# Performance work log

Measured on AMD Instinct MI355X. Metric: run time of the kernel, lower is better.

## Reference

```python
import jax, jax.numpy as jnp
import numpy as np

N = 100000   # total nodes (batched graphs)
E = 800000   # random edges (self-loops appended -> E+N total)
G = 2000     # number of graphs in batch
H = 4        # heads per GAT layer
D = 64       # hidden_size (per-head out dim)
IN = 64      # in_feats
EXTRA = 8    # extra graph-level feats
HID = H * D  # 256


def setup_inputs() -> dict:
    key = jax.random.key(0)
    ks = jax.random.split(key, 24)
    s = 0.5  # init std used in the torch module
    feats_node = jax.random.normal(ks[0], (N, IN), jnp.float32)
    feats_graph = jax.random.normal(ks[1], (G, EXTRA), jnp.float32)
    # edges + self loops (DGL GATConv requires no zero-in-degree nodes)
    src = jnp.concatenate([jax.random.randint(ks[2], (E,), 0, N), jnp.arange(N)])
    dst = jnp.concatenate([jax.random.randint(ks[3], (E,), 0, N), jnp.arange(N)])
    node_gid = jnp.sort(jax.random.randint(ks[4], (N,), 0, G))
    # GAT layer 1
    W1 = jax.random.normal(ks[5], (IN, HID), jnp.float32) * s
    al1 = jax.random.normal(ks[6], (H, D), jnp.float32) * s
    ar1 = jax.random.normal(ks[7], (H, D), jnp.float32) * s
    b1 = jnp.zeros((HID,), jnp.float32)
    # GAT layer 2
    W2 = jax.random.normal(ks[8], (HID, HID), jnp.float32) * s
    al2 = jax.random.normal(ks[9], (H, D), jnp.float32) * s
    ar2 = jax.random.normal(ks[10], (H, D), jnp.float32) * s
    b2 = jnp.zeros((HID,), jnp.float32)
    # WeightedAverage readout score
    Ws = jax.random.normal(ks[11], (HID, 1), jnp.float32) * s
    bs = jnp.zeros((1,), jnp.float32)
    # MLP: 264 -> 128 -> 64 -> 1 with SELU
    Wm1 = jax.random.normal(ks[12], (HID + EXTRA, 2 * D), jnp.float32) * s
    bm1 = jnp.zeros((2 * D,), jnp.float32)
    Wm2 = jax.random.normal(ks[13], (2 * D, D), jnp.float32) * s
    bm2 = jnp.zeros((D,), jnp.float32)
    Wm3 = jax.random.normal(ks[14], (D, 1), jnp.float32) * s
    bm3 = jnp.zeros((1,), jnp.float32)
    return dict(feats_node=feats_node, feats_graph=feats_graph,
                W1=W1, al1=al1, ar1=ar1, b1=b1,
                W2=W2, al2=al2, ar2=ar2, b2=b2,
                Ws=Ws, bs=bs, Wm1=Wm1, bm1=bm1, Wm2=Wm2, bm2=bm2,
                Wm3=Wm3, bm3=bm3,
                src=src, dst=dst, node_gid=node_gid)


def gat_layer(x, W, al, ar, b, src, dst):
    # DGL GATConv: fc -> per-node attn projections -> edge leaky_relu ->
    # edge softmax over incoming edges -> weighted scatter-sum -> +bias
    f = (x @ W).reshape(N, H, D)                       # [N,H,D]
    el = jnp.einsum('nhd,hd->nh', f, al)               # [N,H]
    er = jnp.einsum('nhd,hd->nh', f, ar)               # [N,H]
    e = jax.nn.leaky_relu(el[src] + er[dst], 0.2)      # [E',H]
    m = jax.ops.segment_max(e, dst, num_segments=N)    # per-dst max
    e = jnp.exp(e - m[dst])
    denom = jax.ops.segment_sum(e, dst, num_segments=N)
    alpha = e / denom[dst]                             # edge softmax [E',H]
    out = jax.ops.segment_sum(alpha[:, :, None] * f[src], dst, num_segments=N)
    return out.reshape(N, HID) + b


def reference(feats_node, feats_graph, W1, al1, ar1, b1, W2, al2, ar2, b2,
              Ws, bs, Wm1, bm1, Wm2, bm2, Wm3, bm3, src, dst, node_gid):
    x = jax.nn.relu(gat_layer(feats_node, W1, al1, ar1, b1, src, dst))
    x = jax.nn.relu(gat_layer(x, W2, al2, ar2, b2, src, dst))
    # weighted-average readout per graph: sum(w*x)/sum(w)
    w = jax.nn.sigmoid(x @ Ws + bs)                    # [N,1]
    num = jax.ops.segment_sum(w * x, node_gid, num_segments=G)
    den = jax.ops.segment_sum(w, node_gid, num_segments=G)
    emb = num / jnp.where(den == 0, 1.0, den)          # [G,HID]
    h = jnp.concatenate([emb, feats_graph], axis=1)    # [G,HID+EXTRA]
    h = jax.nn.selu(h @ Wm1 + bm1)
    h = jax.nn.selu(h @ Wm2 + bm2)
    return h @ Wm3 + bm3                               # [G,1]
```

## Files before the change

### kernel.cpp

```cpp
#include <hip/hip_runtime.h>
#include <hip/hip_bf16.h>
#include <math.h>

#define NN     100000
#define GG     2000
#define HH     4
#define DD     64
#define HID    256
#define INF_   64
#define EXTRA  8

typedef unsigned short u16;
typedef __attribute__((ext_vector_type(8))) short bf16x8;
typedef __attribute__((ext_vector_type(4))) float f32x4;

__device__ __forceinline__ u16 f2bf(float f) {
    unsigned u = __float_as_uint(f);
    return (u16)((u + 0x7fffu + ((u >> 16) & 1u)) >> 16);
}
__device__ __forceinline__ float bf2f(u16 v) {
    return __uint_as_float(((unsigned)v) << 16);
}

__global__ __launch_bounds__(256) void wsplit_kernel(
    const float* __restrict__ W, u16* __restrict__ hi, u16* __restrict__ lo,
    int K, int lgK)
{
    int idx = blockIdx.x * 256 + threadIdx.x;
    if (idx >= 256 * K) return;
    int n = idx >> lgK, k = idx & (K - 1);
    float w = W[k * HID + n];
    u16 h = f2bf(w);
    hi[idx] = h;
    lo[idx] = f2bf(w - bf2f(h));
}

__global__ __launch_bounds__(256) void walprep_kernel(
    const float* __restrict__ W1, const float* __restrict__ al,
    const float* __restrict__ ar, float* __restrict__ wal, float* __restrict__ war)
{
    int tid = threadIdx.x;
    int d = tid >> 2, h = tid & 3;
    const float* wrow = W1 + d * HID + h * DD;
    const float* av = al + h * DD;
    const float* bv = ar + h * DD;
    float s1 = 0.f, s2 = 0.f;
    for (int c = 0; c < DD; ++c) { s1 += wrow[c] * av[c]; s2 += wrow[c] * bv[c]; }
    wal[d * 4 + h] = s1;
    war[d * 4 + h] = s2;
}

__global__ __launch_bounds__(256) void elr1_kernel(
    const float* __restrict__ feats, const float* __restrict__ wal,
    const float* __restrict__ war, float* __restrict__ el, float* __restrict__ er)
{
    int idx = blockIdx.x * 256 + threadIdx.x;
    if (idx >= NN * HH) return;
    int n = idx >> 2, h = idx & 3;
    const float* f = feats + (size_t)n * INF_;
    float s1 = 0.f, s2 = 0.f;
    #pragma unroll 4
    for (int d = 0; d < INF_; d += 4) {
        float4 fv = *reinterpret_cast<const float4*>(f + d);
        s1 += fv.x * wal[(d + 0) * 4 + h] + fv.y * wal[(d + 1) * 4 + h]
            + fv.z * wal[(d + 2) * 4 + h] + fv.w * wal[(d + 3) * 4 + h];
        s2 += fv.x * war[(d + 0) * 4 + h] + fv.y * war[(d + 1) * 4 + h]
            + fv.z * war[(d + 2) * 4 + h] + fv.w * war[(d + 3) * 4 + h];
    }
    el[idx] = s1;
    er[idx] = s2;
}

__global__ __launch_bounds__(256) void aggregate_feats_kernel(
    const float* __restrict__ feats, const float* __restrict__ w,
    const float* __restrict__ invden, const int* __restrict__ rowptr,
    const int* __restrict__ colsrc, float* __restrict__ Y1)
{
    int t = blockIdx.x * 4 + (threadIdx.x >> 6);
    int lane = threadIdx.x & 63;
    if (t >= NN) return;
    int beg = rowptr[t], end = rowptr[t + 1];
    float a0 = 0.f, a1 = 0.f, a2 = 0.f, a3 = 0.f;
    float b0 = 0.f, b1 = 0.f, b2 = 0.f, b3 = 0.f;
    int i = beg;
    for (; i + 1 < end; i += 2) {
        int s0 = colsrc[i], s1 = colsrc[i + 1];
        float4 w0 = *reinterpret_cast<const float4*>(w + (size_t)i * 4);
        float4 w1 = *reinterpret_cast<const float4*>(w + (size_t)(i + 1) * 4);
        float f0 = feats[(size_t)s0 * INF_ + lane];
        float f1 = feats[(size_t)s1 * INF_ + lane];
        a0 += w0.x * f0; a1 += w0.y * f0; a2 += w0.z * f0; a3 += w0.w * f0;
        b0 += w1.x * f1; b1 += w1.y * f1; b2 += w1.z * f1; b3 += w1.w * f1;
    }
    if (i < end) {
        int s0 = colsrc[i];
        float4 w0 = *reinterpret_cast<const float4*>(w + (size_t)i * 4);
        float f0 = feats[(size_t)s0 * INF_ + lane];
        a0 += w0.x * f0; a1 += w0.y * f0; a2 += w0.z * f0; a3 += w0.w * f0;
    }
    float4 inv = *reinterpret_cast<const float4*>(invden + (size_t)t * 4);
    float* y = Y1 + (size_t)t * HID;
    y[lane]       = (a0 + b0) * inv.x;
    y[64 + lane]  = (a1 + b1) * inv.y;
    y[128 + lane] = (a2 + b2) * inv.z;
    y[192 + lane] = (a3 + b3) * inv.w;
}

__global__ __launch_bounds__(256) void gemm_head_kernel(
    const float* __restrict__ Y1, const u16* __restrict__ BThi,
    const u16* __restrict__ BTlo, const float* __restrict__ bias,
    u16* __restrict__ Xh, u16* __restrict__ Xl, int M)
{
    const int tid  = threadIdx.x;
    const int wv   = tid >> 6, lane = tid & 63;
    const int quad = lane >> 4, l15 = lane & 15;
    const int r0 = blockIdx.x * 128;
    const int cbase = wv * 64;

    f32x4 acc[8][4];
    #pragma unroll
    for (int i = 0; i < 8; ++i)
        #pragma unroll
        for (int j = 0; j < 4; ++j)
            acc[i][j] = (f32x4){0.f, 0.f, 0.f, 0.f};

    #pragma unroll
    for (int k0 = 0; k0 < 64; k0 += 32) {
        bf16x8 bh[4], bl[4];
        #pragma unroll
        for (int j = 0; j < 4; ++j) {
            int n = cbase + j * 16 + l15;
            bh[j] = *reinterpret_cast<const bf16x8*>(BThi + (size_t)n * 64 + k0 + quad * 8);
            bl[j] = *reinterpret_cast<const bf16x8*>(BTlo + (size_t)n * 64 + k0 + quad * 8);
        }
        #pragma unroll
        for (int i = 0; i < 8; ++i) {
            int gr = min(r0 + i * 16 + l15, M - 1);
            const float* ap = Y1 + (size_t)gr * HID + cbase + k0 + quad * 8;
            float4 va0 = *reinterpret_cast<const float4*>(ap);
            float4 va1 = *reinterpret_cast<const float4*>(ap + 4);
            float av[8] = {va0.x, va0.y, va0.z, va0.w, va1.x, va1.y, va1.z, va1.w};
            bf16x8 vh, vl;
            #pragma unroll
            for (int m = 0; m < 8; ++m) {
                u16 h = f2bf(av[m]);
                vh[m] = (short)h;
                vl[m] = (short)f2bf(av[m] - bf2f(h));
            }
            #pragma unroll
            for (int j = 0; j < 4; ++j) {
                acc[i][j] = __builtin_amdgcn_mfma_f32_16x16x32_bf16(vh, bh[j], acc[i][j], 0, 0, 0);
                acc[i][j] = __builtin_amdgcn_mfma_f32_16x16x32_bf16(vl, bh[j], acc[i][j], 0, 0, 0);
                acc[i][j] = __builtin_amdgcn_mfma_f32_16x16x32_bf16(vh, bl[j], acc[i][j], 0, 0, 0);
            }
        }
    }
    float bv[4];
    #pragma unroll
    for (int j = 0; j < 4; ++j) bv[j] = bias[cbase + j * 16 + l15];
    #pragma unroll
    for (int i = 0; i < 8; ++i)
        #pragma unroll
        for (int rr = 0; rr < 4; ++rr) {
            int grow = r0 + i * 16 + quad * 4 + rr;
            if (grow < M) {
                size_t base = (size_t)grow * HID + cbase + l15;
                #pragma unroll
                for (int j = 0; j < 4; ++j) {
                    float x = fmaxf(acc[i][j][rr] + bv[j], 0.f);
                    u16 h = f2bf(x);
                    Xh[base + j * 16] = h;
                    Xl[base + j * 16] = f2bf(x - bf2f(h));
                }
            }
        }
}

__global__ __launch_bounds__(256) void mfma_gemm_kernel(
    const u16* __restrict__ Ahg, const u16* __restrict__ Alg,
    const u16* __restrict__ BThi, const u16* __restrict__ BTlo,
    u16* __restrict__ Cb,
    const float* __restrict__ al, const float* __restrict__ ar,
    float* __restrict__ el, float* __restrict__ er, int M, int K)
{
    __shared__ __align__(16) u16 Ah[128 * 40];
    __shared__ __align__(16) u16 Al[128 * 40];
    __shared__ __align__(16) u16 Bh[128 * 40];
    __shared__ __align__(16) u16 Bl[128 * 40];
    const int tid  = threadIdx.x;
    const int wave = tid >> 6, lane = tid & 63;
    const int quad = lane >> 4, l15 = lane & 15;
    const int wy = wave >> 1, wx = wave & 1;
    const int r0 = blockIdx.x * 128, c0 = blockIdx.y * 128;
    const int sr = tid >> 2, sseg = tid & 3;

    f32x4 acc[4][4];
    #pragma unroll
    for (int i = 0; i < 4; ++i)
        #pragma unroll
        for (int j = 0; j < 4; ++j)
            acc[i][j] = (f32x4){0.f, 0.f, 0.f, 0.f};

    for (int k0 = 0; k0 < K; k0 += 32) {
        #pragma unroll
        for (int half = 0; half < 2; ++half) {
            int r = sr + half * 64;
            int gr = min(r0 + r, M - 1);
            size_t aoff = (size_t)gr * K + k0 + sseg * 8;
            *reinterpret_cast<bf16x8*>(&Ah[r * 40 + sseg * 8]) =
                *reinterpret_cast<const bf16x8*>(Ahg + aoff);
            *reinterpret_cast<bf16x8*>(&Al[r * 40 + sseg * 8]) =
                *reinterpret_cast<const bf16x8*>(Alg + aoff);
            int gc = c0 + r;
            size_t boff = (size_t)gc * K + k0 + sseg * 8;
            *reinterpret_cast<bf16x8*>(&Bh[r * 40 + sseg * 8]) =
                *reinterpret_cast<const bf16x8*>(BThi + boff);
            *reinterpret_cast<bf16x8*>(&Bl[r * 40 + sseg * 8]) =
                *reinterpret_cast<const bf16x8*>(BTlo + boff);
        }
        __syncthreads();
        bf16x8 afh[4], afl[4], bfh[4], bfl[4];
        #pragma unroll
        for (int i = 0; i < 4; ++i) {
            int row = (wy * 64 + i * 16 + l15) * 40 + quad * 8;
            afh[i] = *reinterpret_cast<const bf16x8*>(&Ah[row]);
            afl[i] = *reinterpret_cast<const bf16x8*>(&Al[row]);
        }
        #pragma unroll
        for (int j = 0; j < 4; ++j) {
            int row = (wx * 64 + j * 16 + l15) * 40 + quad * 8;
            bfh[j] = *reinterpret_cast<const bf16x8*>(&Bh[row]);
            bfl[j] = *reinterpret_cast<const bf16x8*>(&Bl[row]);
        }
        #pragma unroll
        for (int i = 0; i < 4; ++i)
            #pragma unroll
            for (int j = 0; j < 4; ++j) {
                acc[i][j] = __builtin_amdgcn_mfma_f32_16x16x32_bf16(afh[i], bfh[j], acc[i][j], 0, 0, 0);
                acc[i][j] = __builtin_amdgcn_mfma_f32_16x16x32_bf16(afl[i], bfh[j], acc[i][j], 0, 0, 0);
                acc[i][j] = __builtin_amdgcn_mfma_f32_16x16x32_bf16(afh[i], bfl[j], acc[i][j], 0, 0, 0);
            }
        __syncthreads();
    }

    #pragma unroll
    for (int i = 0; i < 4; ++i)
        #pragma unroll
        for (int rr = 0; rr < 4; ++rr) {
            int grow = r0 + wy * 64 + i * 16 + quad * 4 + rr;
            if (grow < M) {
                u16* crow = Cb + (size_t)grow * HID + c0 + wx * 64 + l15;
                #pragma unroll
                for (int j = 0; j < 4; ++j) crow[j * 16] = f2bf(acc[i][j][rr]);
            }
        }

    const int h = blockIdx.y * 2 + wx;
    float alf[4], arf[4];
    #pragma unroll
    for (int j = 0; j < 4; ++j) {
        alf[j] = al[h * DD + j * 16 + l15];
        arf[j] = ar[h * DD + j * 16 + l15];
    }
    #pragma unroll
    for (int i = 0; i < 4; ++i)
        #pragma unroll
        for (int rr = 0; rr < 4; ++rr) {
            float sl = acc[i][0][rr] * alf[0] + acc[i][1][rr] * alf[1]
                     + acc[i][2][rr] * alf[2] + acc[i][3][rr] * alf[3];
            float sr_ = acc[i][0][rr] * arf[0] + acc[i][1][rr] * arf[1]
                      + acc[i][2][rr] * arf[2] + acc[i][3][rr] * arf[3];
            #pragma unroll
            for (int off = 1; off < 16; off <<= 1) {
                sl  += __shfl_xor(sl, off, 64);
                sr_ += __shfl_xor(sr_, off, 64);
            }
            if (l15 == 0) {
                int grow = r0 + wy * 64 + i * 16 + quad * 4 + rr;
                if (grow < M) {
                    el[grow * 4 + h] = sl;
                    er[grow * 4 + h] = sr_;
                }
            }
        }
}

__device__ __forceinline__ float leaky02(float x) { return x > 0.f ? x : 0.2f * x; }

__global__ __launch_bounds__(256) void edge_softmax_kernel(
    const float* __restrict__ el, const float* __restrict__ er,
    const int* __restrict__ rowptr, const int* __restrict__ colsrc,
    float* __restrict__ w, float* __restrict__ invden)
{
    int idx = blockIdx.x * 256 + threadIdx.x;
    if (idx >= NN * HH) return;
    int t = idx >> 2, h = idx & 3;
    int beg = rowptr[t], end = rowptr[t + 1];
    float ert = er[idx];
    float m = -1e30f;
    for (int i = beg; i < end; ++i) {
        int s = colsrc[i];
        m = fmaxf(m, leaky02(el[s * 4 + h] + ert));
    }
    float den = 0.f;
    for (int i = beg; i < end; ++i) {
        int s = colsrc[i];
        float v = expf(leaky02(el[s * 4 + h] + ert) - m);
        w[(size_t)i * 4 + h] = v;
        den += v;
    }
    invden[idx] = 1.f / den;
}

__global__ __launch_bounds__(256) void aggregate_bf16_kernel(
    const u16* __restrict__ F, const float* __restrict__ w,
    const float* __restrict__ invden, const int* __restrict__ rowptr,
    const int* __restrict__ colsrc, const float* __restrict__ bias,
    u16* __restrict__ out)
{
    int t = blockIdx.x * 4 + (threadIdx.x >> 6);
    int lane = threadIdx.x & 63;
    if (t >= NN) return;
    int beg = rowptr[t], end = rowptr[t + 1];
    const int h = lane >> 4;
    float4 acc0 = make_float4(0.f, 0.f, 0.f, 0.f);
    float4 acc1 = make_float4(0.f, 0.f, 0.f, 0.f);
    int i = beg;
    for (; i + 1 < end; i += 2) {
        int s0 = colsrc[i], s1 = colsrc[i + 1];
        float w0 = w[(size_t)i * 4 + h];
        float w1 = w[(size_t)(i + 1) * 4 + h];
        ushort4 f0 = *reinterpret_cast<const ushort4*>(F + (size_t)s0 * HID + 4 * lane);
        ushort4 f1 = *reinterpret_cast<const ushort4*>(F + (size_t)s1 * HID + 4 * lane);
        acc0.x += w0 * bf2f(f0.x); acc0.y += w0 * bf2f(f0.y);
        acc0.z += w0 * bf2f(f0.z); acc0.w += w0 * bf2f(f0.w);
        acc1.x += w1 * bf2f(f1.x); acc1.y += w1 * bf2f(f1.y);
        acc1.z += w1 * bf2f(f1.z); acc1.w += w1 * bf2f(f1.w);
    }
    if (i < end) {
        int s0 = colsrc[i];
        float w0 = w[(size_t)i * 4 + h];
        ushort4 f0 = *reinterpret_cast<const ushort4*>(F + (size_t)s0 * HID + 4 * lane);
        acc0.x += w0 * bf2f(f0.x); acc0.y += w0 * bf2f(f0.y);
        acc0.z += w0 * bf2f(f0.z); acc0.w += w0 * bf2f(f0.w);
    }
    float inv = invden[t * 4 + h];
    float4 bv = *reinterpret_cast<const float4*>(bias + 4 * lane);
    ushort4 r;
    r.x = f2bf(fmaxf((acc0.x + acc1.x) * inv + bv.x, 0.f));
    r.y = f2bf(fmaxf((acc0.y + acc1.y) * inv + bv.y, 0.f));
    r.z = f2bf(fmaxf((acc0.z + acc1.z) * inv + bv.z, 0.f));
    r.w = f2bf(fmaxf((acc0.w + acc1.w) * inv + bv.w, 0.f));
    *reinterpret_cast<ushort4*>(out + (size_t)t * HID + 4 * lane) = r;
}

__global__ __launch_bounds__(256) void readout_kernel(
    const u16* __restrict__ X, const float* __restrict__ Ws,
    const float* __restrict__ bs, const int* __restrict__ gptr,
    float* __restrict__ emb)
{
    int g = blockIdx.x * 4 + (threadIdx.x >> 6);
    int lane = threadIdx.x & 63;
    if (g >= GG) return;
    int beg = gptr[g], end = gptr[g + 1];
    float4 wv = *reinterpret_cast<const float4*>(Ws + 4 * lane);
    float b = bs[0];
    float4 acc = make_float4(0.f, 0.f, 0.f, 0.f);
    float wsum = 0.f;
    for (int n = beg; n < end; ++n) {
        ushort4 xv = *reinterpret_cast<const ushort4*>(X + (size_t)n * HID + 4 * lane);
        float x0 = bf2f(xv.x), x1 = bf2f(xv.y), x2 = bf2f(xv.z), x3 = bf2f(xv.w);
        float p = x0 * wv.x + x1 * wv.y + x2 * wv.z + x3 * wv.w;
        #pragma unroll
        for (int off = 32; off; off >>= 1) p += __shfl_xor(p, off, 64);
        float w = 1.f / (1.f + expf(-(p + b)));
        wsum += w;
        acc.x += w * x0; acc.y += w * x1; acc.z += w * x2; acc.w += w * x3;
    }
    float inv = (wsum == 0.f) ? 1.f : wsum;
    float4 e;
    e.x = acc.x / inv; e.y = acc.y / inv; e.z = acc.z / inv; e.w = acc.w / inv;
    *reinterpret_cast<float4*>(emb + (size_t)g * HID + 4 * lane) = e;
}

__device__ __forceinline__ float selu_f(float x)
{
    const float scale = 1.0507009873554805f, alpha = 1.6732632423543772f;
    return scale * (x > 0.f ? x : alpha * expm1f(x));
}

__global__ __launch_bounds__(128) void mlp_kernel(
    const float* __restrict__ emb, const float* __restrict__ fg,
    const float* __restrict__ Wm1, const float* __restrict__ bm1,
    const float* __restrict__ Wm2, const float* __restrict__ bm2,
    const float* __restrict__ Wm3, const float* __restrict__ bm3,
    float* __restrict__ out)
{
    int g = blockIdx.x;
    __shared__ float h[HID + EXTRA];
    __shared__ float h1[128];
    __shared__ float h2[64];
    int tid = threadIdx.x;
    h[tid] = emb[(size_t)g * HID + tid];
    h[128 + tid] = emb[(size_t)g * HID + 128 + tid];
    if (tid < EXTRA) h[HID + tid] = fg[(size_t)g * EXTRA + tid];
    __syncthreads();
    float acc = bm1[tid];
    for (int i = 0; i < HID + EXTRA; ++i) acc += h[i] * Wm1[i * 128 + tid];
    h1[tid] = selu_f(acc);
    __syncthreads();
    if (tid < 64) {
        float acc2 = bm2[tid];
        for (int i = 0; i < 128; ++i) acc2 += h1[i] * Wm2[i * 64 + tid];
        h2[tid] = selu_f(acc2);
    }
    __syncthreads();
    if (tid < 64) {
        float p = h2[tid] * Wm3[tid];
        #pragma unroll
        for (int off = 32; off; off >>= 1) p += __shfl_xor(p, off, 64);
        if (tid == 0) out[g] = p + bm3[0];
    }
}

__global__ void count_dst_kernel(const int* __restrict__ dst, int* __restrict__ cnt, int E)
{
    int e = blockIdx.x * 256 + threadIdx.x;
    if (e < E) atomicAdd(&cnt[dst[e]], 1);
}
__global__ void count_gid_kernel(const int* __restrict__ gid, int* __restrict__ cnt, int n)
{
    int i = blockIdx.x * 256 + threadIdx.x;
    if (i < n) atomicAdd(&cnt[gid[i]], 1);
}
__global__ void fill_csr_kernel(const int* __restrict__ src, const int* __restrict__ dst,
                                int* __restrict__ cursor, int* __restrict__ colsrc, int E)
{
    int e = blockIdx.x * 256 + threadIdx.x;
    if (e < E) {
        int p = atomicAdd(&cursor[dst[e]], 1);
        colsrc[p] = src[e];
    }
}

__global__ __launch_bounds__(256) void scan_blocks_kernel(
    const int* __restrict__ in, int n, int* __restrict__ out, int* __restrict__ partials)
{
    __shared__ int lds[256];
    int tid = threadIdx.x;
    int base = blockIdx.x * 1024 + tid * 4;
    int v0 = (base + 0 < n) ? in[base + 0] : 0;
    int v1 = (base + 1 < n) ? in[base + 1] : 0;
    int v2 = (base + 2 < n) ? in[base + 2] : 0;
    int v3 = (base + 3 < n) ? in[base + 3] : 0;
    int s = v0 + v1 + v2 + v3;
    lds[tid] = s;
    __syncthreads();
    for (int off = 1; off < 256; off <<= 1) {
        int t = (tid >= off) ? lds[tid - off] : 0;
        __syncthreads();
        lds[tid] += t;
        __syncthreads();
    }
    int excl = lds[tid] - s;
    if (base + 0 < n) out[base + 0] = excl;
    if (base + 1 < n) out[base + 1] = excl + v0;
    if (base + 2 < n) out[base + 2] = excl + v0 + v1;
    if (base + 3 < n) out[base + 3] = excl + v0 + v1 + v2;
    if (tid == 255) partials[blockIdx.x] = lds[255];
}

__global__ __launch_bounds__(256) void scan_partials_kernel(int* partials, int nb)
{
    __shared__ int lds[256];
    int tid = threadIdx.x;
    int v = (tid < nb) ? partials[tid] : 0;
    lds[tid] = v;
    __syncthreads();
    for (int off = 1; off < 256; off <<= 1) {
        int t = (tid >= off) ? lds[tid - off] : 0;
        __syncthreads();
        lds[tid] += t;
        __syncthreads();
    }
    int excl = lds[tid] - v;
    if (tid < nb) partials[tid] = excl;
}

__global__ void add_offsets_kernel(int* __restrict__ out, const int* __restrict__ partials, int n)
{
    int i = blockIdx.x * 256 + threadIdx.x;
    if (i < n) out[i] += partials[i >> 10];
}

extern "C" void kernel_launch(void* const* d_in, const int* in_sizes, int n_in,
                              void* d_out, int out_size, void* d_ws, size_t ws_size,
                              hipStream_t stream)
{
    const float* feats_node  = (const float*)d_in[0];
    const float* feats_graph = (const float*)d_in[1];
    const float* W1  = (const float*)d_in[2];
    const float* al1 = (const float*)d_in[3];
    const float* ar1 = (const float*)d_in[4];
    const float* b1  = (const float*)d_in[5];
    const float* W2  = (const float*)d_in[6];
    const float* al2 = (const float*)d_in[7];
    const float* ar2 = (const float*)d_in[8];
    const float* b2  = (const float*)d_in[9];
    const float* Ws  = (const float*)d_in[10];
    const float* bs  = (const float*)d_in[11];
    const float* Wm1 = (const float*)d_in[12];
    const float* bm1 = (const float*)d_in[13];
    const float* Wm2 = (const float*)d_in[14];
    const float* bm2 = (const float*)d_in[15];
    const float* Wm3 = (const float*)d_in[16];
    const float* bm3 = (const float*)d_in[17];
    const int* src = (const int*)d_in[18];
    const int* dst = (const int*)d_in[19];
    const int* gid = (const int*)d_in[20];
    float* out = (float*)d_out;
    const int E = in_sizes[18];

    char* p = (char*)d_ws;
    auto alloc = [&](size_t bytes) {
        char* r = p;
        p += (bytes + 255) & ~(size_t)255;
        return r;
    };
    float* Y1     = (float*)alloc((size_t)NN * HID * 4);
    u16*   Xh     = (u16*)alloc((size_t)NN * HID * 2);
    u16*   Xl     = (u16*)alloc((size_t)NN * HID * 2);
    float* el     = (float*)alloc((size_t)NN * HH * 4);
    float* er     = (float*)alloc((size_t)NN * HH * 4);
    float* wbuf   = (float*)alloc((size_t)E * HH * 4);
    float* invden = (float*)alloc((size_t)NN * HH * 4);
    int*   cnt    = (int*)alloc((size_t)(NN + 1) * 4);
    int*   rowptr = (int*)alloc((size_t)(NN + 1) * 4);
    int*   colsrc = (int*)alloc((size_t)E * 4);
    int*   gcnt   = (int*)alloc((size_t)(GG + 1) * 4);
    int*   gptr   = (int*)alloc((size_t)(GG + 1) * 4);
    int*   parts  = (int*)alloc(1024 * 4);
    float* emb    = (float*)alloc((size_t)GG * HID * 4);
    u16*   BT1h   = (u16*)alloc((size_t)HID * INF_ * 2);
    u16*   BT1l   = (u16*)alloc((size_t)HID * INF_ * 2);
    u16*   BT2h   = (u16*)alloc((size_t)HID * HID * 2);
    u16*   BT2l   = (u16*)alloc((size_t)HID * HID * 2);
    float* wal1   = (float*)alloc(INF_ * HH * 4);
    float* war1   = (float*)alloc(INF_ * HH * 4);
    u16*   Fbf2   = (u16*)Y1;
    u16*   Xbf2   = Xh;

    hipMemsetAsync(cnt, 0, (size_t)(NN + 1) * 4, stream);
    count_dst_kernel<<<(E + 255) / 256, 256, 0, stream>>>(dst, cnt, E);
    {
        int n = NN + 1, nb = (n + 1023) / 1024;
        scan_blocks_kernel<<<nb, 256, 0, stream>>>(cnt, n, rowptr, parts);
        scan_partials_kernel<<<1, 256, 0, stream>>>(parts, nb);
        add_offsets_kernel<<<(n + 255) / 256, 256, 0, stream>>>(rowptr, parts, n);
    }
    hipMemcpyAsync(cnt, rowptr, (size_t)(NN + 1) * 4, hipMemcpyDeviceToDevice, stream);
    fill_csr_kernel<<<(E + 255) / 256, 256, 0, stream>>>(src, dst, cnt, colsrc, E);

    hipMemsetAsync(gcnt, 0, (size_t)(GG + 1) * 4, stream);
    count_gid_kernel<<<(NN + 255) / 256, 256, 0, stream>>>(gid, gcnt, NN);
    {
        int n = GG + 1, nb = (n + 1023) / 1024;
        scan_blocks_kernel<<<nb, 256, 0, stream>>>(gcnt, n, gptr, parts);
        scan_partials_kernel<<<1, 256, 0, stream>>>(parts, nb);
        add_offsets_kernel<<<(n + 255) / 256, 256, 0, stream>>>(gptr, parts, n);
    }

    wsplit_kernel<<<(HID * INF_ + 255) / 256, 256, 0, stream>>>(W1, BT1h, BT1l, INF_, 6);
    wsplit_kernel<<<(HID * HID + 255) / 256, 256, 0, stream>>>(W2, BT2h, BT2l, HID, 8);
    walprep_kernel<<<1, 256, 0, stream>>>(W1, al1, ar1, wal1, war1);

    const int nh_blocks = (NN * HH + 255) / 256;

    elr1_kernel<<<nh_blocks, 256, 0, stream>>>(feats_node, wal1, war1, el, er);
    edge_softmax_kernel<<<nh_blocks, 256, 0, stream>>>(el, er, rowptr, colsrc, wbuf, invden);
    aggregate_feats_kernel<<<(NN + 3) / 4, 256, 0, stream>>>(feats_node, wbuf, invden,
                                                             rowptr, colsrc, Y1);
    gemm_head_kernel<<<(NN + 127) / 128, 256, 0, stream>>>(Y1, BT1h, BT1l, b1, Xh, Xl, NN);

    dim3 ggrid((NN + 127) / 128, HID / 128);
    mfma_gemm_kernel<<<ggrid, 256, 0, stream>>>(
        Xh, Xl, BT2h, BT2l, Fbf2, al2, ar2, el, er, NN, HID);
    edge_softmax_kernel<<<nh_blocks, 256, 0, stream>>>(el, er, rowptr, colsrc, wbuf, invden);
    aggregate_bf16_kernel<<<(NN + 3) / 4, 256, 0, stream>>>(Fbf2, wbuf, invden, rowptr, colsrc,
                                                            b2, Xbf2);

    readout_kernel<<<(GG + 3) / 4, 256, 0, stream>>>(Xbf2, Ws, bs, gptr, emb);
    mlp_kernel<<<GG, 128, 0, stream>>>(emb, feats_graph, Wm1, bm1, Wm2, bm2, Wm3, bm3, out);
}
```

Measured before the change: 655.6 us.

## Emit bf16 hi/lo from aggregation and tile layer-1 head GEMM via LDS

The first-layer aggregation now writes its per-head output directly as bf16 hi/lo split arrays instead of fp32, so the split happens once at the producer. The head GEMM now launches one block per (row tile, head), stages the A and B tiles in padded shared memory and splits the work across a 2x2 wave grid. Previously each wave re-read fp32 rows and re-split them in registers. This cuts global bytes and redundant conversion work, at the cost of LDS staging, a barrier and four times as many blocks.

```diff
diff --git a/kernel.cpp b/kernel.cpp
--- a/kernel.cpp
+++ b/kernel.cpp
@@ -74,7 +74,7 @@
 __global__ __launch_bounds__(256) void aggregate_feats_kernel(
     const float* __restrict__ feats, const float* __restrict__ w,
     const float* __restrict__ invden, const int* __restrict__ rowptr,
-    const int* __restrict__ colsrc, float* __restrict__ Y1)
+    const int* __restrict__ colsrc, u16* __restrict__ Yh, u16* __restrict__ Yl)
 {
     int t = blockIdx.x * 4 + (threadIdx.x >> 6);
     int lane = threadIdx.x & 63;
@@ -99,74 +99,107 @@
         a0 += w0.x * f0; a1 += w0.y * f0; a2 += w0.z * f0; a3 += w0.w * f0;
     }
     float4 inv = *reinterpret_cast<const float4*>(invden + (size_t)t * 4);
-    float* y = Y1 + (size_t)t * HID;
-    y[lane]       = (a0 + b0) * inv.x;
-    y[64 + lane]  = (a1 + b1) * inv.y;
-    y[128 + lane] = (a2 + b2) * inv.z;
-    y[192 + lane] = (a3 + b3) * inv.w;
-}
-
+    float y0 = (a0 + b0) * inv.x;
+    float y1 = (a1 + b1) * inv.y;
+    float y2 = (a2 + b2) * inv.z;
+    float y3 = (a3 + b3) * inv.w;
+    u16* yh = Yh + (size_t)t * HID;
+    u16* yl = Yl + (size_t)t * HID;
+    u16 h0 = f2bf(y0), h1 = f2bf(y1), h2 = f2bf(y2), h3 = f2bf(y3);
+    yh[lane] = h0;        yl[lane] = f2bf(y0 - bf2f(h0));
+    yh[64 + lane] = h1;   yl[64 + lane] = f2bf(y1 - bf2f(h1));
+    yh[128 + lane] = h2;  yl[128 + lane] = f2bf(y2 - bf2f(h2));
+    yh[192 + lane] = h3;  yl[192 + lane] = f2bf(y3 - bf2f(h3));
+}
+
+#define GH_STRIDE 72
 __global__ __launch_bounds__(256) void gemm_head_kernel(
-    const float* __restrict__ Y1, const u16* __restrict__ BThi,
-    const u16* __restrict__ BTlo, const float* __restrict__ bias,
+    const u16* __restrict__ Yh, const u16* __restrict__ Yl,
+    const u16* __restrict__ BThi, const u16* __restrict__ BTlo,
+    const float* __restrict__ bias,
     u16* __restrict__ Xh, u16* __restrict__ Xl, int M)
 {
+    __shared__ __align__(16) u16 Ah[128 * GH_STRIDE];
+    __shared__ __align__(16) u16 Al[128 * GH_STRIDE];
+    __shared__ __align__(16) u16 Bh[64 * GH_STRIDE];
+    __shared__ __align__(16) u16 Bl[64 * GH_STRIDE];
     const int tid  = threadIdx.x;
-    const int wv   = tid >> 6, lane = tid & 63;
+    const int wave = tid >> 6, lane = tid & 63;
     const int quad = lane >> 4, l15 = lane & 15;
+    const int wy = wave >> 1, wx = wave & 1;
+    const int head = blockIdx.y;
     const int r0 = blockIdx.x * 128;
-    const int cbase = wv * 64;
-
-    f32x4 acc[8][4];
-    #pragma unroll
-    for (int i = 0; i < 8; ++i)
-        #pragma unroll
-        for (int j = 0; j < 4; ++j)
+    const int cb = head * DD;
+
+    {
+        int row = tid >> 1, half = tid & 1;
+        int gr = min(r0 + row, M - 1);
+        size_t goff = (size_t)gr * HID + cb + half * 32;
+        int loff = row * GH_STRIDE + half * 32;
+        #pragma unroll
+        for (int m = 0; m < 4; ++m) {
+            *reinterpret_cast<bf16x8*>(&Ah[loff + m * 8]) =
+                *reinterpret_cast<const bf16x8*>(Yh + goff + m * 8);
+            *reinterpret_cast<bf16x8*>(&Al[loff + m * 8]) =
+                *reinterpret_cast<const bf16x8*>(Yl + goff + m * 8);
+        }
+        int d = tid & 63, seg = tid >> 6;
+        size_t boff = (size_t)(head * DD + d) * 64 + seg * 16;
+        int bloff = d * GH_STRIDE + seg * 16;
+        #pragma unroll
+        for (int m = 0; m < 2; ++m) {
+            *reinterpret_cast<bf16x8*>(&Bh[bloff + m * 8]) =
+                *reinterpret_cast<const bf16x8*>(BThi + boff + m * 8);
+            *reinterpret_cast<bf16x8*>(&Bl[bloff + m * 8]) =
+                *reinterpret_cast<const bf16x8*>(BTlo + boff + m * 8);
+        }
+    }
+    __syncthreads();
+
+    f32x4 acc[4][2];
+    #pragma unroll
+    for (int i = 0; i < 4; ++i)
+        #pragma unroll
+        for (int j = 0; j < 2; ++j)
             acc[i][j] = (f32x4){0.f, 0.f, 0.f, 0.f};
 
     #pragma unroll
     for (int k0 = 0; k0 < 64; k0 += 32) {
-        bf16x8 bh[4], bl[4];
-        #pragma unroll
-        for (int j = 0; j < 4; ++j) {
-            int n = cbase + j * 16 + l15;
-            bh[j] = *reinterpret_cast<const bf16x8*>(BThi + (size_t)n * 64 + k0 + quad * 8);
-            bl[j] = *reinterpret_cast<const bf16x8*>(BTlo + (size_t)n * 64 + k0 + quad * 8);
-        }
-        #pragma unroll
-        for (int i = 0; i < 8; ++i) {
-            int gr = min(r0 + i * 16 + l15, M - 1);
-            const float* ap = Y1 + (size_t)gr * HID + cbase + k0 + quad * 8;
-            float4 va0 = *reinterpret_cast<const float4*>(ap);
-            float4 va1 = *reinterpret_cast<const float4*>(ap + 4);
-            float av[8] = {va0.x, va0.y, va0.z, va0.w, va1.x, va1.y, va1.z, va1.w};
-            bf16x8 vh, vl;
+        bf16x8 afh[4], afl[4], bfh[2], bfl[2];
+        #pragma unroll
+        for (int i = 0; i < 4; ++i) {
+            int row = (wy * 64 + i * 16 + l15) * GH_STRIDE + k0 + quad * 8;
+            afh[i] = *reinterpret_cast<const bf16x8*>(&Ah[row]);
+            afl[i] = *reinterpret_cast<const bf16x8*>(&Al[row]);
+        }
+        #pragma unroll
+        for (int j = 0; j < 2; ++j) {
+            int row = (wx * 32 + j * 16 + l15) * GH_STRIDE + k0 + quad * 8;
+            bfh[j] = *reinterpret_cast<const bf16x8*>(&Bh[row]);
+            bfl[j] = *reinterpret_cast<const bf16x8*>(&Bl[row]);
+        }
+        #pragma unroll
+        for (int i = 0; i < 4; ++i)
             #pragma unroll
-            for (int m = 0; m < 8; ++m) {
-                u16 h = f2bf(av[m]);
-                vh[m] = (short)h;
-                vl[m] = (short)f2bf(av[m] - bf2f(h));
+            for (int j = 0; j < 2; ++j) {
+                acc[i][j] = __builtin_amdgcn_mfma_f32_16x16x32_bf16(afh[i], bfh[j], acc[i][j], 0, 0, 0);
+                acc[i][j] = __builtin_amdgcn_mfma_f32_16x16x32_bf16(afl[i], bfh[j], acc[i][j], 0, 0, 0);
+                acc[i][j] = __builtin_amdgcn_mfma_f32_16x16x32_bf16(afh[i], bfl[j], acc[i][j], 0, 0, 0);
             }
-            #pragma unroll
-            for (int j = 0; j < 4; ++j) {
-                acc[i][j] = __builtin_amdgcn_mfma_f32_16x16x32_bf16(vh, bh[j], acc[i][j], 0, 0, 0);
-                acc[i][j] = __builtin_amdgcn_mfma_f32_16x16x32_bf16(vl, bh[j], acc[i][j], 0, 0, 0);
-                acc[i][j] = __builtin_amdgcn_mfma_f32_16x16x32_bf16(vh, bl[j], acc[i][j], 0, 0, 0);
-            }
-        }
-    }
-    float bv[4];
-    #pragma unroll
-    for (int j = 0; j < 4; ++j) bv[j] = bias[cbase + j * 16 + l15];
-    #pragma unroll
-    for (int i = 0; i < 8; ++i)
+    }
+
+    float bv[2];
+    #pragma unroll
+    for (int j = 0; j < 2; ++j) bv[j] = bias[cb + wx * 32 + j * 16 + l15];
+    #pragma unroll
+    for (int i = 0; i < 4; ++i)
         #pragma unroll
         for (int rr = 0; rr < 4; ++rr) {
-            int grow = r0 + i * 16 + quad * 4 + rr;
+            int grow = r0 + wy * 64 + i * 16 + quad * 4 + rr;
             if (grow < M) {
-                size_t base = (size_t)grow * HID + cbase + l15;
+                size_t base = (size_t)grow * HID + cb + wx * 32 + l15;
                 #pragma unroll
-                for (int j = 0; j < 4; ++j) {
+                for (int j = 0; j < 2; ++j) {
                     float x = fmaxf(acc[i][j][rr] + bv[j], 0.f);
                     u16 h = f2bf(x);
                     Xh[base + j * 16] = h;
@@ -527,7 +560,8 @@
         p += (bytes + 255) & ~(size_t)255;
         return r;
     };
-    float* Y1     = (float*)alloc((size_t)NN * HID * 4);
+    u16*   Yh     = (u16*)alloc((size_t)NN * HID * 2);
+    u16*   Yl     = (u16*)alloc((size_t)NN * HID * 2);
     u16*   Xh     = (u16*)alloc((size_t)NN * HID * 2);
     u16*   Xl     = (u16*)alloc((size_t)NN * HID * 2);
     float* el     = (float*)alloc((size_t)NN * HH * 4);
@@ -547,7 +581,7 @@
     u16*   BT2l   = (u16*)alloc((size_t)HID * HID * 2);
     float* wal1   = (float*)alloc(INF_ * HH * 4);
     float* war1   = (float*)alloc(INF_ * HH * 4);
-    u16*   Fbf2   = (u16*)Y1;
+    u16*   Fbf2   = Yh;
     u16*   Xbf2   = Xh;
 
     hipMemsetAsync(cnt, 0, (size_t)(NN + 1) * 4, stream);
@@ -579,8 +613,11 @@
     elr1_kernel<<<nh_blocks, 256, 0, stream>>>(feats_node, wal1, war1, el, er);
     edge_softmax_kernel<<<nh_blocks, 256, 0, stream>>>(el, er, rowptr, colsrc, wbuf, invden);
     aggregate_feats_kernel<<<(NN + 3) / 4, 256, 0, stream>>>(feats_node, wbuf, invden,
-                                                             rowptr, colsrc, Y1);
-    gemm_head_kernel<<<(NN + 127) / 128, 256, 0, stream>>>(Y1, BT1h, BT1l, b1, Xh, Xl, NN);
+                                                             rowptr, colsrc, Yh, Yl);
+    {
+        dim3 hgrid((NN + 127) / 128, HH);
+        gemm_head_kernel<<<hgrid, 256, 0, stream>>>(Yh, Yl, BT1h, BT1l, b1, Xh, Xl, NN);
+    }
 
     dim3 ggrid((NN + 127) / 128, HID / 128);
     mfma_gemm_kernel<<<ggrid, 256, 0, stream>>>(
```

Measured after the change: 637.6 us. 1.03x faster.
